# Optimization experiments

Hardware: AMD Instinct MI355X
Metric: run time of the kernel (lower is better)

Reference implementation:

```python
import jax, jax.numpy as jnp
import numpy as np
import math

B, N, E, H, DEPTH, MLP_RATIO, A = 8, 1024, 768, 12, 6, 4, 7
F = MLP_RATIO * E


def _get_attention_slopes(n):
    def p2(n):
        start = 2 ** (-2 ** (-(math.log2(n) - 3)))
        return [start * start ** i for i in range(n)]
    if math.log2(n).is_integer():
        return p2(n)
    c = 2 ** math.floor(math.log2(n))
    return p2(c) + _get_attention_slopes(2 * c)[0::2][: n - c]


def _ln(x, scale, bias, eps=1e-6):
    m = jnp.mean(x, axis=-1, keepdims=True)
    v = jnp.var(x, axis=-1, keepdims=True)
    return (x - m) * jax.lax.rsqrt(v + eps) * scale + bias


def setup_inputs() -> dict:
    key = jax.random.key(0)
    ks = jax.random.split(key, 8)
    s = 0.02
    return {
        "x": jax.random.normal(ks[0], (B, N, E), jnp.float32),
        "ln1_scale": jnp.ones((DEPTH, E), jnp.float32),
        "ln1_bias": jnp.zeros((DEPTH, E), jnp.float32),
        "wqkv": jax.random.normal(ks[1], (DEPTH, E, 3 * E), jnp.float32) * s,
        "bqkv": jnp.zeros((DEPTH, 3 * E), jnp.float32),
        "wo": jax.random.normal(ks[2], (DEPTH, E, E), jnp.float32) * s,
        "bo": jnp.zeros((DEPTH, E), jnp.float32),
        "ln2_scale": jnp.ones((DEPTH, E), jnp.float32),
        "ln2_bias": jnp.zeros((DEPTH, E), jnp.float32),
        "w1": jax.random.normal(ks[3], (DEPTH, E, F), jnp.float32) * s,
        "w2": jax.random.normal(ks[4], (DEPTH, F, E), jnp.float32) * s,
        "lnf_scale": jnp.ones((E,), jnp.float32),
        "lnf_bias": jnp.zeros((E,), jnp.float32),
        "head_w1": jax.random.normal(ks[5], (E, E), jnp.float32) * s,
        "head_b1": jnp.zeros((E,), jnp.float32),
        "head_w2": jax.random.normal(ks[6], (E, A), jnp.float32) * s,
    }


def reference(x, ln1_scale, ln1_bias, wqkv, bqkv, wo, bo, ln2_scale, ln2_bias, w1, w2, lnf_scale, lnf_bias, head_w1, head_b1, head_w2):
    b, n, e = x.shape
    h = H
    dh = e // h
    scale = dh ** (-0.5)
    # ALiBi bias: slopes[h] * key-position (exactly as original code computes it)
    slopes = jnp.asarray(_get_attention_slopes(h), x.dtype)
    pos_bias = slopes[None, :, None, None] * jnp.arange(n, dtype=x.dtype)[None, None, None, :]
    causal = jnp.tril(jnp.ones((n, n), bool))[None, None]  # [1,1,n,n]
    big_neg = jnp.finfo(x.dtype).min

    depth = ln1_scale.shape[0]
    for i in range(depth):
        y = _ln(x, ln1_scale[i], ln1_bias[i])
        qkv = y @ wqkv[i] + bqkv[i]
        q, k, v = jnp.split(qkv, 3, axis=-1)
        q = q.reshape(b, n, h, dh).transpose(0, 2, 1, 3)  # b h n d
        k = k.reshape(b, n, h, dh).transpose(0, 2, 1, 3)
        v = v.reshape(b, n, h, dh).transpose(0, 2, 1, 3)
        att = jnp.einsum('bhnd,bhmd->bhnm', q, k) * scale + pos_bias
        att = jnp.where(causal, att, big_neg)
        att = jax.nn.softmax(att, axis=-1)
        o = jnp.einsum('bhnm,bhmd->bhnd', att, v)
        o = o.transpose(0, 2, 1, 3).reshape(b, n, e)
        x = x + (o @ wo[i] + bo[i])
        y = _ln(x, ln2_scale[i], ln2_bias[i])
        y = jax.nn.gelu(y @ w1[i])  # flax default: tanh-approx gelu; FF has no bias
        x = x + y @ w2[i]
    x = _ln(x, lnf_scale, lnf_bias)
    actions = jax.nn.relu(x @ head_w1 + head_b1) @ head_w2
    return actions
```

## Files before the change

### kernel.cpp

```cpp
#include <hip/hip_runtime.h>
#include <hip/hip_bf16.h>
#include <cstdint>

#define DEV __device__ __forceinline__

typedef __bf16 bf16x8 __attribute__((ext_vector_type(8)));
typedef float f32x4 __attribute__((ext_vector_type(4)));
typedef unsigned short u16;
typedef u16 u16x8 __attribute__((ext_vector_type(8)));
typedef u16 u16x4 __attribute__((ext_vector_type(4)));
typedef uint32_t u32x2 __attribute__((ext_vector_type(2)));
typedef uint32_t u32x4 __attribute__((ext_vector_type(4)));

DEV u16 f2bf(float f) {
  union { float f; uint32_t u; } a; a.f = f;
  uint32_t u = a.u + 0x7fffu + ((a.u >> 16) & 1u);
  return (u16)(u >> 16);
}
DEV float b2f(u16 v) {
  union { uint32_t u; float f; } a; a.u = ((uint32_t)v) << 16;
  return a.f;
}

DEV float fexp2(float x) {
#if __has_builtin(__builtin_amdgcn_exp2f)
  return __builtin_amdgcn_exp2f(x);
#else
  return __expf(x * 0.69314718056f);
#endif
}

DEV uint32_t cvtpk(float lo, float hi) {
  uint32_t r;
  asm("v_cvt_pk_bf16_f32 %0, %1, %2" : "=v"(r) : "v"(lo), "v"(hi));
  return r;
}

DEV void gload16(const void* g, void* lds) {
  __builtin_amdgcn_global_load_lds((__attribute__((address_space(1))) void*)g,
                                   (__attribute__((address_space(3))) void*)lds,
                                   16, 0, 0);
}

struct TMat { const float* src; u16* dst; int K; int N; int t0; };
struct TArgs { TMat m[26]; int nmat; };

__global__ __launch_bounds__(256) void transpose_all(TArgs args) {
  __shared__ float tile[64][65];
  const int bid = blockIdx.x;
  int i = 0;
  #pragma unroll 1
  for (int t = 1; t < args.nmat; ++t) if (bid >= args.m[t].t0) i = t;
  const TMat mm = args.m[i];
  const int tid = bid - mm.t0;
  const int ntx = mm.N >> 6;
  const int tx = tid % ntx, ty = tid / ntx;
  const int n0 = tx * 64, k0 = ty * 64;
  const int c = threadIdx.x & 63, r0 = threadIdx.x >> 6;
  #pragma unroll
  for (int s = 0; s < 16; ++s) {
    int r = r0 + s * 4;
    tile[r][c] = mm.src[(size_t)(k0 + r) * mm.N + n0 + c];
  }
  __syncthreads();
  #pragma unroll
  for (int s = 0; s < 16; ++s) {
    int rr = r0 + s * 4;
    mm.dst[(size_t)(n0 + rr) * mm.K + k0 + c] = f2bf(tile[c][rr]);
  }
}

__global__ __launch_bounds__(256) void f2b_kernel(const float4* __restrict__ in,
                                                  u32x4* __restrict__ out, int n8) {
  const int i = blockIdx.x * 256 + threadIdx.x;
  if (i >= n8) return;
  float4 a = in[2 * i], b = in[2 * i + 1];
  u32x4 o;
  o[0] = cvtpk(a.x, a.y); o[1] = cvtpk(a.z, a.w);
  o[2] = cvtpk(b.x, b.y); o[3] = cvtpk(b.z, b.w);
  out[i] = o;
}

__global__ __launch_bounds__(256) void ln_kernel(const u16* __restrict__ x,
                                                 const float* __restrict__ sc,
                                                 const float* __restrict__ bi,
                                                 u16* __restrict__ y, int Mtok) {
  const int bid = blockIdx.x;
  const int tok = ((bid & 7) << 10) + ((bid >> 3) << 2) + (threadIdx.x >> 6);
  const int l = threadIdx.x & 63;
  if (tok >= Mtok) return;
  const u16* row = x + (size_t)tok * 768;
  u16x8 v0 = *(const u16x8*)(row + l * 8);
  u16x4 v1 = *(const u16x4*)(row + 512 + l * 4);
  float f[12];
  #pragma unroll
  for (int i = 0; i < 8; ++i) f[i] = b2f(v0[i]);
  #pragma unroll
  for (int i = 0; i < 4; ++i) f[8 + i] = b2f(v1[i]);
  float s = 0.f, q = 0.f;
  #pragma unroll
  for (int i = 0; i < 12; ++i) { s += f[i]; q += f[i] * f[i]; }
  #pragma unroll
  for (int off = 1; off < 64; off <<= 1) { s += __shfl_xor(s, off); q += __shfl_xor(q, off); }
  const float mean = s * (1.f / 768.f);
  const float var = q * (1.f / 768.f) - mean * mean;
  const float r = rsqrtf(var + 1e-6f);
  float4 s0 = *(const float4*)(sc + l * 8);
  float4 s1 = *(const float4*)(sc + l * 8 + 4);
  float4 s2 = *(const float4*)(sc + 512 + l * 4);
  float4 b0 = *(const float4*)(bi + l * 8);
  float4 b1 = *(const float4*)(bi + l * 8 + 4);
  float4 b2 = *(const float4*)(bi + 512 + l * 4);
  float g[12];
  g[0] = (f[0]-mean)*r*s0.x + b0.x;  g[1] = (f[1]-mean)*r*s0.y + b0.y;
  g[2] = (f[2]-mean)*r*s0.z + b0.z;  g[3] = (f[3]-mean)*r*s0.w + b0.w;
  g[4] = (f[4]-mean)*r*s1.x + b1.x;  g[5] = (f[5]-mean)*r*s1.y + b1.y;
  g[6] = (f[6]-mean)*r*s1.z + b1.z;  g[7] = (f[7]-mean)*r*s1.w + b1.w;
  g[8] = (f[8]-mean)*r*s2.x + b2.x;  g[9] = (f[9]-mean)*r*s2.y + b2.y;
  g[10] = (f[10]-mean)*r*s2.z + b2.z; g[11] = (f[11]-mean)*r*s2.w + b2.w;
  u16* yr = y + (size_t)tok * 768;
  u32x4 o;
  o[0] = cvtpk(g[0], g[1]); o[1] = cvtpk(g[2], g[3]);
  o[2] = cvtpk(g[4], g[5]); o[3] = cvtpk(g[6], g[7]);
  *(u32x4*)(yr + l * 8) = o;
  u32x2 o2; o2[0] = cvtpk(g[8], g[9]); o2[1] = cvtpk(g[10], g[11]);
  *(u32x2*)(yr + 512 + l * 4) = o2;
}

enum { EPI_BF16 = 0, EPI_RESID = 1, EPI_GELU = 2, EPI_RELU = 3 };

__global__ __launch_bounds__(256, 2) void gemm128(
    const u16* __restrict__ A, const u16* __restrict__ Bt,
    const float* __restrict__ bias, const u16* __restrict__ residB,
    u16* __restrict__ outB, int N, int K, int nxb, int epi) {
  __shared__ u16 smem[32768];
  const int tid = threadIdx.x;
  const int w = tid >> 6, l = tid & 63;

  const int nwg = gridDim.x;
  const int flat = blockIdx.x;
  const int wg = (flat & 7) * (nwg >> 3) + (flat >> 3);
  const int bx = wg % nxb, by = wg / nxb;
  const int m0 = by << 7, n0 = bx << 7;

  const int wr = (w >> 1) << 6, wc = (w & 1) << 6;
  const int cl = l & 15, g = l >> 4;
  f32x4 acc[4][4] = {};

  const int lrow = l >> 3;
  const int scol = ((l & 7) ^ lrow) << 3;
  const u16* agp = A  + (size_t)(m0 + (w << 5) + lrow) * K + scol;
  const u16* bgp = Bt + (size_t)(n0 + (w << 5) + lrow) * K + scol;
  const int ldso = w << 11;
  const int nkt = K >> 6;

  #pragma unroll
  for (int q = 0; q < 4; ++q) {
    gload16(agp + (size_t)(q * 8) * K, &smem[ldso + (q << 9)]);
    gload16(bgp + (size_t)(q * 8) * K, &smem[16384 + ldso + (q << 9)]);
  }

  const int sw = cl & 7;
  for (int kt = 0; kt < nkt; ++kt) {
    const int cur = kt & 1;
    if (kt + 1 < nkt) {
      const size_t koff = (size_t)(kt + 1) << 6;
      const int nb = (cur ^ 1) << 13;
      #pragma unroll
      for (int q = 0; q < 4; ++q) {
        gload16(agp + koff + (size_t)(q * 8) * K, &smem[nb + ldso + (q << 9)]);
        gload16(bgp + koff + (size_t)(q * 8) * K, &smem[16384 + nb + ldso + (q << 9)]);
      }
      asm volatile("s_waitcnt vmcnt(8)" ::: "memory");
    } else {
      asm volatile("s_waitcnt vmcnt(0)" ::: "memory");
    }
    __builtin_amdgcn_s_barrier();
    __builtin_amdgcn_sched_barrier(0);
    const u16* Ab = &smem[cur << 13];
    const u16* Bb = &smem[16384 + (cur << 13)];
    #pragma unroll
    for (int ks = 0; ks < 2; ++ks) {
      bf16x8 af[4], bfr[4];
      const int ps = (((ks << 2) | g) ^ sw) << 3;
      #pragma unroll
      for (int mt = 0; mt < 4; ++mt)
        af[mt] = *(const bf16x8*)(Ab + ((wr + mt * 16 + cl) << 6) + ps);
      #pragma unroll
      for (int nt = 0; nt < 4; ++nt)
        bfr[nt] = *(const bf16x8*)(Bb + ((wc + nt * 16 + cl) << 6) + ps);
      #pragma unroll
      for (int mt = 0; mt < 4; ++mt)
        #pragma unroll
        for (int nt = 0; nt < 4; ++nt)
          acc[mt][nt] = __builtin_amdgcn_mfma_f32_16x16x32_bf16(af[mt], bfr[nt], acc[mt][nt], 0, 0, 0);
    }
    asm volatile("s_waitcnt lgkmcnt(0)" ::: "memory");
    __builtin_amdgcn_s_barrier();
  }

  float* scr = (float*)smem + w * 1056;
  const int rg = g << 2;
  const int er = l >> 3;
  const int ec0 = (l & 7) << 3;
  #pragma unroll
  for (int mt = 0; mt < 4; ++mt) {
    #pragma unroll
    for (int nt = 0; nt < 4; ++nt)
      #pragma unroll
      for (int j = 0; j < 4; ++j)
        scr[(rg + j) * 66 + nt * 16 + cl] = acc[mt][nt][j];
    #pragma unroll
    for (int t = 0; t < 2; ++t) {
      const int r = (t << 3) + er;
      const int grow = m0 + wr + mt * 16 + r;
      const int gcol = n0 + wc + ec0;
      float v[8];
      #pragma unroll
      for (int u = 0; u < 8; ++u) v[u] = scr[r * 66 + ec0 + u];
      if (bias) {
        #pragma unroll
        for (int u = 0; u < 8; ++u) v[u] += bias[gcol + u];
      }
      if (epi == EPI_RESID) {
        u16x8 rv = *(const u16x8*)(residB + (size_t)grow * N + gcol);
        #pragma unroll
        for (int u = 0; u < 8; ++u) v[u] += b2f(rv[u]);
      } else if (epi == EPI_GELU) {
        #pragma unroll
        for (int u = 0; u < 8; ++u) {
          const float x = v[u];
          const float e = __expf(-(1.5957691216f * x + 0.0713548163f * x * x * x));
          v[u] = x / (1.f + e);
        }
      } else if (epi == EPI_RELU) {
        #pragma unroll
        for (int u = 0; u < 8; ++u) v[u] = fmaxf(v[u], 0.f);
      }
      u32x4 ov;
      ov[0] = cvtpk(v[0], v[1]); ov[1] = cvtpk(v[2], v[3]);
      ov[2] = cvtpk(v[4], v[5]); ov[3] = cvtpk(v[6], v[7]);
      u32x4* op = (u32x4*)(outB + (size_t)grow * N + gcol);
      if (epi == EPI_BF16 || epi == EPI_GELU)
        __builtin_nontemporal_store(ov, op);
      else
        *op = ov;
    }
  }
}

__global__ __launch_bounds__(512, 2) void attn_kernel(const u16* __restrict__ qkv,
                                                      u16* __restrict__ o) {
  __shared__ u16 Ksm[2][4096];
  __shared__ u16 Vt[2][64][68];
  __shared__ u16 P[8][16][72];
  const int flat = blockIdx.x;
  const int b = flat & 7;
  const int rr = flat >> 3;
  const int h = rr >> 3;
  const int j = rr & 7;
  const int tid = threadIdx.x;
  const int w = tid >> 6, l = tid & 63;
  const int cl = l & 15, lg = l >> 4;
  const int qtile = (w < 4) ? j : 15 - j;
  const int q0 = qtile * 64 + (w & 3) * 16;
  const int rowg = q0 + cl;
  const float log2e = 1.44269504f;
  const float scale2 = 0.125f * log2e;
  const float slope = (h < 8) ? exp2f(-(float)(h + 1)) : exp2f(-0.5f - (float)(h - 8));
  const float slope2 = slope * log2e;
  const size_t rs_ = 2304;
  const size_t bbase = (size_t)b * 1024 * rs_;

  const u16* qp = qkv + bbase + (size_t)rowg * rs_ + h * 64 + lg * 8;
  bf16x8 qa0 = *(const bf16x8*)qp;
  bf16x8 qa1 = *(const bf16x8*)(qp + 32);

  float m_r = -1e30f, l_r = 0.f;
  f32x4 oacc[4];
  #pragma unroll
  for (int d = 0; d < 4; ++d) oacc[d] = (f32x4){0.f, 0.f, 0.f, 0.f};

  const u16* ksrc = qkv + bbase + (size_t)(tid >> 3) * rs_ + 768 + h * 64 +
                    (((tid & 7) ^ ((tid >> 3) & 7)) << 3);
  const int vd0 = w << 3;
  const u16* vbase = qkv + bbase + (size_t)l * rs_ + 1536 + h * 64 + vd0;

  const int nkv = 16 - j;
  gload16(ksrc, &Ksm[0][w << 9]);
  u16x8 vreg = *(const u16x8*)vbase;
  __syncthreads();

  const int sw = cl & 7;
  const int ps0 = (lg ^ sw) << 3;
  const int ps1 = ps0 ^ 32;

  for (int kv = 0; kv < nkv; ++kv) {
    const int buf = kv & 1;
    #pragma unroll
    for (int i = 0; i < 8; ++i) Vt[buf][vd0 + i][l] = vreg[i];
    u16x8 vnext = vreg;
    if (kv + 1 < nkv) {
      gload16(ksrc + (size_t)(kv + 1) * 64 * rs_, &Ksm[buf ^ 1][w << 9]);
      vnext = *(const u16x8*)(vbase + (size_t)(kv + 1) * 64 * rs_);
    }

    const bool active = (kv <= qtile);
    bf16x8 pa0, pa1;
    if (active) {
      const u16* Kb = &Ksm[buf][0];
      f32x4 pp[4];
      float pm = -3.0e38f;
      __builtin_amdgcn_s_setprio(1);
      #pragma unroll
      for (int nt = 0; nt < 4; ++nt) {
        const int row = nt * 16 + cl;
        bf16x8 bk0 = *(const bf16x8*)(Kb + (row << 6) + ps0);
        bf16x8 bk1 = *(const bf16x8*)(Kb + (row << 6) + ps1);
        f32x4 s = (f32x4){0.f, 0.f, 0.f, 0.f};
        s = __builtin_amdgcn_mfma_f32_16x16x32_bf16(bk0, qa0, s, 0, 0, 0);
        s = __builtin_amdgcn_mfma_f32_16x16x32_bf16(bk1, qa1, s, 0, 0, 0);
        const int kb = kv * 64 + nt * 16 + (lg << 2);
        #pragma unroll
        for (int jj = 0; jj < 4; ++jj) {
          const int colg = kb + jj;
          float v = s[jj] * scale2 + slope2 * (float)colg;
          pp[nt][jj] = (colg <= rowg) ? v : -3.0e38f;
        }
        pm = fmaxf(pm, fmaxf(fmaxf(pp[nt][0], pp[nt][1]),
                             fmaxf(pp[nt][2], pp[nt][3])));
      }
      __builtin_amdgcn_s_setprio(0);
      pm = fmaxf(pm, __shfl_xor(pm, 16));
      pm = fmaxf(pm, __shfl_xor(pm, 32));
      if (!__all(pm <= m_r + 11.54f)) {
        const float mnew = fmaxf(m_r, pm);
        const float al = fexp2(m_r - mnew);
        m_r = mnew;
        l_r *= al;
        float a4[4];
        #pragma unroll
        for (int jj = 0; jj < 4; ++jj) a4[jj] = __shfl(al, (lg << 2) + jj);
        #pragma unroll
        for (int d = 0; d < 4; ++d)
          #pragma unroll
          for (int jj = 0; jj < 4; ++jj) oacc[d][jj] *= a4[jj];
      }
      float rs = 0.f;
      #pragma unroll
      for (int nt = 0; nt < 4; ++nt) {
        #pragma unroll
        for (int jj = 0; jj < 4; ++jj) {
          float p = fexp2(pp[nt][jj] - m_r);
          pp[nt][jj] = p;
          rs += p;
        }
      }
      rs += __shfl_xor(rs, 16);
      rs += __shfl_xor(rs, 32);
      l_r += rs;
      #pragma unroll
      for (int nt = 0; nt < 4; ++nt) {
        u32x2 pr;
        pr[0] = cvtpk(pp[nt][0], pp[nt][1]);
        pr[1] = cvtpk(pp[nt][2], pp[nt][3]);
        *(u32x2*)&P[w][cl][nt * 16 + (lg << 2)] = pr;
      }
      pa0 = *(const bf16x8*)&P[w][cl][lg * 8];
      pa1 = *(const bf16x8*)&P[w][cl][32 + lg * 8];
    }

    __syncthreads();

    if (active) {
      __builtin_amdgcn_s_setprio(1);
      #pragma unroll
      for (int d = 0; d < 4; ++d) {
        bf16x8 bv0 = *(const bf16x8*)&Vt[buf][d * 16 + cl][lg * 8];
        bf16x8 bv1 = *(const bf16x8*)&Vt[buf][d * 16 + cl][32 + lg * 8];
        oacc[d] = __builtin_amdgcn_mfma_f32_16x16x32_bf16(pa0, bv0, oacc[d], 0, 0, 0);
        oacc[d] = __builtin_amdgcn_mfma_f32_16x16x32_bf16(pa1, bv1, oacc[d], 0, 0, 0);
      }
      __builtin_amdgcn_s_setprio(0);
    }
    vreg = vnext;
  }

  const float linv = 1.f / l_r;
  float i4[4];
  #pragma unroll
  for (int jj = 0; jj < 4; ++jj) i4[jj] = __shfl(linv, (lg << 2) + jj);
  u16* op = o + ((size_t)b * 1024 + q0) * 768 + h * 64;
  #pragma unroll
  for (int d = 0; d < 4; ++d)
    #pragma unroll
    for (int jj = 0; jj < 4; ++jj)
      op[(size_t)((lg << 2) + jj) * 768 + d * 16 + cl] = f2bf(oacc[d][jj] * i4[jj]);
}

__global__ __launch_bounds__(256) void head2_kernel(const u16* __restrict__ act,
                                                    const float* __restrict__ w,
                                                    float* __restrict__ out, int Mtok) {
  const int bid = blockIdx.x;
  const int tok = ((bid & 7) << 10) + ((bid >> 3) << 2) + (threadIdx.x >> 6);
  const int l = threadIdx.x & 63;
  if (tok >= Mtok) return;
  float s[7] = {0.f, 0.f, 0.f, 0.f, 0.f, 0.f, 0.f};
  const u16* ar = act + (size_t)tok * 768;
  #pragma unroll
  for (int i = 0; i < 12; ++i) {
    const int k = l + i * 64;
    const float a = b2f(ar[k]);
    #pragma unroll
    for (int j = 0; j < 7; ++j) s[j] += a * w[k * 7 + j];
  }
  #pragma unroll
  for (int off = 32; off; off >>= 1)
    #pragma unroll
    for (int j = 0; j < 7; ++j) s[j] += __shfl_down(s[j], off);
  if (l == 0) {
    #pragma unroll
    for (int j = 0; j < 7; ++j) out[(size_t)tok * 7 + j] = s[j];
  }
}

extern "C" void kernel_launch(void* const* d_in, const int* in_sizes, int n_in,
                              void* d_out, int out_size, void* d_ws, size_t ws_size,
                              hipStream_t stream) {
  const float* x_in = (const float*)d_in[0];
  const float* ln1s = (const float*)d_in[1];
  const float* ln1b = (const float*)d_in[2];
  const float* wqkv = (const float*)d_in[3];
  const float* bqkv = (const float*)d_in[4];
  const float* wo   = (const float*)d_in[5];
  const float* bo   = (const float*)d_in[6];
  const float* ln2s = (const float*)d_in[7];
  const float* ln2b = (const float*)d_in[8];
  const float* w1   = (const float*)d_in[9];
  const float* w2   = (const float*)d_in[10];
  const float* lnfs = (const float*)d_in[11];
  const float* lnfb = (const float*)d_in[12];
  const float* hw1  = (const float*)d_in[13];
  const float* hb1  = (const float*)d_in[14];
  const float* hw2  = (const float*)d_in[15];
  float* out = (float*)d_out;

  const int Mtok = 8192, E = 768, E3 = 2304, F = 3072, DEPTH = 6;

  char* ws = (char*)d_ws;
  size_t off = 0;
  auto alloc = [&](size_t bytes) -> char* {
    char* p = ws + off; off += (bytes + 255) & ~(size_t)255; return p;
  };
  u16*  wqkvt = (u16*)alloc((size_t)DEPTH * E3 * E * 2);
  u16*  wot   = (u16*)alloc((size_t)DEPTH * E * E * 2);
  u16*  w1t   = (u16*)alloc((size_t)DEPTH * F * E * 2);
  u16*  w2t   = (u16*)alloc((size_t)DEPTH * E * F * 2);
  u16*  hw1t  = (u16*)alloc((size_t)E * E * 2);
  u16*  xb    = (u16*)alloc((size_t)Mtok * E * 2);
  u16*  yb    = (u16*)alloc((size_t)Mtok * E * 2);
  u16*  big   = (u16*)alloc((size_t)Mtok * F * 2);
  (void)ws_size; (void)in_sizes; (void)n_in; (void)out_size;

  TArgs ta; int nm = 0; int t0 = 0;
  auto add = [&](const float* s, u16* d, int K, int N) {
    ta.m[nm].src = s; ta.m[nm].dst = d; ta.m[nm].K = K; ta.m[nm].N = N; ta.m[nm].t0 = t0;
    t0 += (N / 64) * (K / 64); ++nm;
  };
  for (int i = 0; i < DEPTH; ++i) add(wqkv + (size_t)i * E * E3, wqkvt + (size_t)i * E3 * E, E, E3);
  for (int i = 0; i < DEPTH; ++i) add(wo + (size_t)i * E * E, wot + (size_t)i * E * E, E, E);
  for (int i = 0; i < DEPTH; ++i) add(w1 + (size_t)i * E * F, w1t + (size_t)i * F * E, E, F);
  for (int i = 0; i < DEPTH; ++i) add(w2 + (size_t)i * F * E, w2t + (size_t)i * E * F, F, E);
  add(hw1, hw1t, E, E);
  ta.nmat = nm;
  transpose_all<<<t0, 256, 0, stream>>>(ta);

  f2b_kernel<<<(Mtok * E / 8 + 255) / 256, 256, 0, stream>>>(
      (const float4*)x_in, (u32x4*)xb, Mtok * E / 8);

  u16* qkvb = big;
  for (int i = 0; i < DEPTH; ++i) {
    ln_kernel<<<Mtok / 4, 256, 0, stream>>>(xb, ln1s + i * E, ln1b + i * E, yb, Mtok);
    gemm128<<<18 * 64, 256, 0, stream>>>(yb, wqkvt + (size_t)i * E3 * E, bqkv + (size_t)i * E3,
                                         nullptr, qkvb, E3, E, 18, EPI_BF16);
    attn_kernel<<<768, 512, 0, stream>>>(qkvb, yb);
    gemm128<<<6 * 64, 256, 0, stream>>>(yb, wot + (size_t)i * E * E, bo + (size_t)i * E,
                                        xb, xb, E, E, 6, EPI_RESID);
    ln_kernel<<<Mtok / 4, 256, 0, stream>>>(xb, ln2s + i * E, ln2b + i * E, yb, Mtok);
    gemm128<<<24 * 64, 256, 0, stream>>>(yb, w1t + (size_t)i * F * E, nullptr,
                                         nullptr, big, F, E, 24, EPI_GELU);
    gemm128<<<6 * 64, 256, 0, stream>>>(big, w2t + (size_t)i * E * F, nullptr,
                                        xb, xb, E, F, 6, EPI_RESID);
  }
  ln_kernel<<<Mtok / 4, 256, 0, stream>>>(xb, lnfs, lnfb, yb, Mtok);
  gemm128<<<6 * 64, 256, 0, stream>>>(yb, hw1t, hb1, nullptr, big,
                                      E, E, 6, EPI_RELU);
  head2_kernel<<<Mtok / 4, 256, 0, stream>>>(big, hw2, out, Mtok);
}
```

Measured before the change: 1.410 ms.

## Fold LayerNorm into GEMM epilogues via precomputed weight column sums

Replaces the LayerNorm kernels that wrote normalized bf16 activations with a small row-stats kernel (mean, rstd). The LN scale is folded into the transposed weights, and per-column sums of scaled weights and of bias-weighted weights are computed with atomics during weight preparation. The GEMM then consumes raw x and applies (acc - mean*cs)*rstd + bW in its epilogue. This removes one full activation write and read per LayerNorm, at the cost of numerical differences from mean subtraction after bf16 accumulation and extra atomics in the transpose. The transpose kernel also switches to vectorized float4 loads and packed stores.

```diff
diff --git a/kernel.cpp b/kernel.cpp
--- a/kernel.cpp
+++ b/kernel.cpp
@@ -42,8 +42,9 @@
                                    16, 0, 0);
 }
 
-struct TMat { const float* src; u16* dst; int K; int N; int t0; };
-struct TArgs { TMat m[26]; int nmat; };
+struct TMat { const float* src; u16* dst; float* cs; float* bW;
+              const float* sc; const float* bi; int K; int N; int t0; };
+struct TArgs { TMat m[25]; int nmat; };
 
 __global__ __launch_bounds__(256) void transpose_all(TArgs args) {
   __shared__ float tile[64][65];
@@ -52,21 +53,42 @@
   #pragma unroll 1
   for (int t = 1; t < args.nmat; ++t) if (bid >= args.m[t].t0) i = t;
   const TMat mm = args.m[i];
-  const int tid = bid - mm.t0;
+  const int tid = threadIdx.x;
+  const int tix = bid - mm.t0;
   const int ntx = mm.N >> 6;
-  const int tx = tid % ntx, ty = tid / ntx;
-  const int n0 = tx * 64, k0 = ty * 64;
-  const int c = threadIdx.x & 63, r0 = threadIdx.x >> 6;
-  #pragma unroll
-  for (int s = 0; s < 16; ++s) {
-    int r = r0 + s * 4;
-    tile[r][c] = mm.src[(size_t)(k0 + r) * mm.N + n0 + c];
+  const int n0 = (tix % ntx) << 6, k0 = (tix / ntx) << 6;
+  const int lr = tid >> 4, lc4 = (tid & 15) << 2;
+  #pragma unroll
+  for (int p = 0; p < 4; ++p) {
+    const int r = lr + p * 16;
+    *(float4*)&tile[r][lc4] =
+        *(const float4*)(mm.src + (size_t)(k0 + r) * mm.N + n0 + lc4);
   }
   __syncthreads();
-  #pragma unroll
-  for (int s = 0; s < 16; ++s) {
-    int rr = r0 + s * 4;
-    mm.dst[(size_t)(n0 + rr) * mm.K + k0 + c] = f2bf(tile[c][rr]);
+  if (mm.cs && tid < 64) {
+    float s1 = 0.f, s2 = 0.f;
+    #pragma unroll 1
+    for (int r = 0; r < 64; ++r) {
+      const float v = tile[r][tid];
+      s1 += mm.sc[k0 + r] * v;
+      s2 += mm.bi[k0 + r] * v;
+    }
+    atomicAdd(mm.cs + n0 + tid, s1);
+    atomicAdd(mm.bW + n0 + tid, s2);
+  }
+  const int wn = tid >> 4, wk4 = (tid & 15) << 2;
+  float scv[4];
+  #pragma unroll
+  for (int u = 0; u < 4; ++u) scv[u] = mm.sc ? mm.sc[k0 + wk4 + u] : 1.f;
+  #pragma unroll
+  for (int p = 0; p < 4; ++p) {
+    const int n = wn + p * 16;
+    const float v0 = tile[wk4][n] * scv[0];
+    const float v1 = tile[wk4 + 1][n] * scv[1];
+    const float v2 = tile[wk4 + 2][n] * scv[2];
+    const float v3 = tile[wk4 + 3][n] * scv[3];
+    u32x2 o; o[0] = cvtpk(v0, v1); o[1] = cvtpk(v2, v3);
+    *(u32x2*)(mm.dst + (size_t)(n0 + n) * mm.K + k0 + wk4) = o;
   }
 }
 
@@ -81,10 +103,8 @@
   out[i] = o;
 }
 
-__global__ __launch_bounds__(256) void ln_kernel(const u16* __restrict__ x,
-                                                 const float* __restrict__ sc,
-                                                 const float* __restrict__ bi,
-                                                 u16* __restrict__ y, int Mtok) {
+__global__ __launch_bounds__(256) void rowstats(const u16* __restrict__ x,
+                                                float2* __restrict__ rs, int Mtok) {
   const int bid = blockIdx.x;
   const int tok = ((bid & 7) << 10) + ((bid >> 3) << 2) + (threadIdx.x >> 6);
   const int l = threadIdx.x & 63;
@@ -92,47 +112,29 @@
   const u16* row = x + (size_t)tok * 768;
   u16x8 v0 = *(const u16x8*)(row + l * 8);
   u16x4 v1 = *(const u16x4*)(row + 512 + l * 4);
-  float f[12];
-  #pragma unroll
-  for (int i = 0; i < 8; ++i) f[i] = b2f(v0[i]);
-  #pragma unroll
-  for (int i = 0; i < 4; ++i) f[8 + i] = b2f(v1[i]);
   float s = 0.f, q = 0.f;
   #pragma unroll
-  for (int i = 0; i < 12; ++i) { s += f[i]; q += f[i] * f[i]; }
+  for (int i = 0; i < 8; ++i) { float f = b2f(v0[i]); s += f; q += f * f; }
+  #pragma unroll
+  for (int i = 0; i < 4; ++i) { float f = b2f(v1[i]); s += f; q += f * f; }
   #pragma unroll
   for (int off = 1; off < 64; off <<= 1) { s += __shfl_xor(s, off); q += __shfl_xor(q, off); }
-  const float mean = s * (1.f / 768.f);
-  const float var = q * (1.f / 768.f) - mean * mean;
-  const float r = rsqrtf(var + 1e-6f);
-  float4 s0 = *(const float4*)(sc + l * 8);
-  float4 s1 = *(const float4*)(sc + l * 8 + 4);
-  float4 s2 = *(const float4*)(sc + 512 + l * 4);
-  float4 b0 = *(const float4*)(bi + l * 8);
-  float4 b1 = *(const float4*)(bi + l * 8 + 4);
-  float4 b2 = *(const float4*)(bi + 512 + l * 4);
-  float g[12];
-  g[0] = (f[0]-mean)*r*s0.x + b0.x;  g[1] = (f[1]-mean)*r*s0.y + b0.y;
-  g[2] = (f[2]-mean)*r*s0.z + b0.z;  g[3] = (f[3]-mean)*r*s0.w + b0.w;
-  g[4] = (f[4]-mean)*r*s1.x + b1.x;  g[5] = (f[5]-mean)*r*s1.y + b1.y;
-  g[6] = (f[6]-mean)*r*s1.z + b1.z;  g[7] = (f[7]-mean)*r*s1.w + b1.w;
-  g[8] = (f[8]-mean)*r*s2.x + b2.x;  g[9] = (f[9]-mean)*r*s2.y + b2.y;
-  g[10] = (f[10]-mean)*r*s2.z + b2.z; g[11] = (f[11]-mean)*r*s2.w + b2.w;
-  u16* yr = y + (size_t)tok * 768;
-  u32x4 o;
-  o[0] = cvtpk(g[0], g[1]); o[1] = cvtpk(g[2], g[3]);
-  o[2] = cvtpk(g[4], g[5]); o[3] = cvtpk(g[6], g[7]);
-  *(u32x4*)(yr + l * 8) = o;
-  u32x2 o2; o2[0] = cvtpk(g[8], g[9]); o2[1] = cvtpk(g[10], g[11]);
-  *(u32x2*)(yr + 512 + l * 4) = o2;
-}
-
-enum { EPI_BF16 = 0, EPI_RESID = 1, EPI_GELU = 2, EPI_RELU = 3 };
+  if (l == 0) {
+    const float mean = s * (1.f / 768.f);
+    const float var = q * (1.f / 768.f) - mean * mean;
+    float2 o; o.x = mean; o.y = rsqrtf(var + 1e-6f);
+    rs[tok] = o;
+  }
+}
+
+enum { EPI_LN = 0, EPI_RESID = 1, EPI_LNGELU = 2, EPI_LNRELU = 3 };
 
 __global__ __launch_bounds__(256, 2) void gemm128(
     const u16* __restrict__ A, const u16* __restrict__ Bt,
     const float* __restrict__ bias, const u16* __restrict__ residB,
-    u16* __restrict__ outB, int N, int K, int nxb, int epi) {
+    u16* __restrict__ outB, const float2* __restrict__ rstat,
+    const float* __restrict__ cs, const float* __restrict__ bW,
+    int N, int K, int nxb, int epi) {
   __shared__ u16 smem[32768];
   const int tid = threadIdx.x;
   const int w = tid >> 6, l = tid & 63;
@@ -218,30 +220,34 @@
       float v[8];
       #pragma unroll
       for (int u = 0; u < 8; ++u) v[u] = scr[r * 66 + ec0 + u];
-      if (bias) {
-        #pragma unroll
-        for (int u = 0; u < 8; ++u) v[u] += bias[gcol + u];
-      }
       if (epi == EPI_RESID) {
+        if (bias) {
+          #pragma unroll
+          for (int u = 0; u < 8; ++u) v[u] += bias[gcol + u];
+        }
         u16x8 rv = *(const u16x8*)(residB + (size_t)grow * N + gcol);
         #pragma unroll
         for (int u = 0; u < 8; ++u) v[u] += b2f(rv[u]);
-      } else if (epi == EPI_GELU) {
+      } else {
+        const float2 st = rstat[grow];
         #pragma unroll
         for (int u = 0; u < 8; ++u) {
-          const float x = v[u];
-          const float e = __expf(-(1.5957691216f * x + 0.0713548163f * x * x * x));
-          v[u] = x / (1.f + e);
+          float x = (v[u] - st.x * cs[gcol + u]) * st.y + bW[gcol + u];
+          if (bias) x += bias[gcol + u];
+          if (epi == EPI_LNGELU) {
+            const float e = __expf(-(1.5957691216f * x + 0.0713548163f * x * x * x));
+            x = x / (1.f + e);
+          } else if (epi == EPI_LNRELU) {
+            x = fmaxf(x, 0.f);
+          }
+          v[u] = x;
         }
-      } else if (epi == EPI_RELU) {
-        #pragma unroll
-        for (int u = 0; u < 8; ++u) v[u] = fmaxf(v[u], 0.f);
       }
       u32x4 ov;
       ov[0] = cvtpk(v[0], v[1]); ov[1] = cvtpk(v[2], v[3]);
       ov[2] = cvtpk(v[4], v[5]); ov[3] = cvtpk(v[6], v[7]);
       u32x4* op = (u32x4*)(outB + (size_t)grow * N + gcol);
-      if (epi == EPI_BF16 || epi == EPI_GELU)
+      if (epi == EPI_LN || epi == EPI_LNGELU)
         __builtin_nontemporal_store(ov, op);
       else
         *op = ov;
@@ -457,21 +463,40 @@
   u16*  w1t   = (u16*)alloc((size_t)DEPTH * F * E * 2);
   u16*  w2t   = (u16*)alloc((size_t)DEPTH * E * F * 2);
   u16*  hw1t  = (u16*)alloc((size_t)E * E * 2);
+  const int ncs = DEPTH * E3 * 2 + DEPTH * F * 2 + E * 2;
+  float* csbuf = (float*)alloc((size_t)ncs * 4);
+  float* csq = csbuf;            float* bWq = csq + DEPTH * E3;
+  float* csw = bWq + DEPTH * E3; float* bWw = csw + DEPTH * F;
+  float* csh = bWw + DEPTH * F;  float* bWh = csh + E;
+  float2* rs = (float2*)alloc((size_t)Mtok * 8);
   u16*  xb    = (u16*)alloc((size_t)Mtok * E * 2);
   u16*  yb    = (u16*)alloc((size_t)Mtok * E * 2);
   u16*  big   = (u16*)alloc((size_t)Mtok * F * 2);
   (void)ws_size; (void)in_sizes; (void)n_in; (void)out_size;
 
+  hipMemsetAsync(csbuf, 0, (size_t)ncs * 4, stream);
+
   TArgs ta; int nm = 0; int t0 = 0;
-  auto add = [&](const float* s, u16* d, int K, int N) {
-    ta.m[nm].src = s; ta.m[nm].dst = d; ta.m[nm].K = K; ta.m[nm].N = N; ta.m[nm].t0 = t0;
+  auto add = [&](const float* s, u16* d, int K, int N,
+                 float* cs, float* bW, const float* sc, const float* bi) {
+    ta.m[nm].src = s; ta.m[nm].dst = d; ta.m[nm].cs = cs; ta.m[nm].bW = bW;
+    ta.m[nm].sc = sc; ta.m[nm].bi = bi; ta.m[nm].K = K; ta.m[nm].N = N;
+    ta.m[nm].t0 = t0;
     t0 += (N / 64) * (K / 64); ++nm;
   };
-  for (int i = 0; i < DEPTH; ++i) add(wqkv + (size_t)i * E * E3, wqkvt + (size_t)i * E3 * E, E, E3);
-  for (int i = 0; i < DEPTH; ++i) add(wo + (size_t)i * E * E, wot + (size_t)i * E * E, E, E);
-  for (int i = 0; i < DEPTH; ++i) add(w1 + (size_t)i * E * F, w1t + (size_t)i * F * E, E, F);
-  for (int i = 0; i < DEPTH; ++i) add(w2 + (size_t)i * F * E, w2t + (size_t)i * E * F, F, E);
-  add(hw1, hw1t, E, E);
+  for (int i = 0; i < DEPTH; ++i)
+    add(wqkv + (size_t)i * E * E3, wqkvt + (size_t)i * E3 * E, E, E3,
+        csq + i * E3, bWq + i * E3, ln1s + i * E, ln1b + i * E);
+  for (int i = 0; i < DEPTH; ++i)
+    add(wo + (size_t)i * E * E, wot + (size_t)i * E * E, E, E,
+        nullptr, nullptr, nullptr, nullptr);
+  for (int i = 0; i < DEPTH; ++i)
+    add(w1 + (size_t)i * E * F, w1t + (size_t)i * F * E, E, F,
+        csw + i * F, bWw + i * F, ln2s + i * E, ln2b + i * E);
+  for (int i = 0; i < DEPTH; ++i)
+    add(w2 + (size_t)i * F * E, w2t + (size_t)i * E * F, F, E,
+        nullptr, nullptr, nullptr, nullptr);
+  add(hw1, hw1t, E, E, csh, bWh, lnfs, lnfb);
   ta.nmat = nm;
   transpose_all<<<t0, 256, 0, stream>>>(ta);
 
@@ -480,20 +505,28 @@
 
   u16* qkvb = big;
   for (int i = 0; i < DEPTH; ++i) {
-    ln_kernel<<<Mtok / 4, 256, 0, stream>>>(xb, ln1s + i * E, ln1b + i * E, yb, Mtok);
-    gemm128<<<18 * 64, 256, 0, stream>>>(yb, wqkvt + (size_t)i * E3 * E, bqkv + (size_t)i * E3,
-                                         nullptr, qkvb, E3, E, 18, EPI_BF16);
+    rowstats<<<Mtok / 4, 256, 0, stream>>>(xb, rs, Mtok);
+    gemm128<<<18 * 64, 256, 0, stream>>>(xb, wqkvt + (size_t)i * E3 * E,
+                                         bqkv + (size_t)i * E3, nullptr, qkvb,
+                                         rs, csq + i * E3, bWq + i * E3,
+                                         E3, E, 18, EPI_LN);
     attn_kernel<<<768, 512, 0, stream>>>(qkvb, yb);
-    gemm128<<<6 * 64, 256, 0, stream>>>(yb, wot + (size_t)i * E * E, bo + (size_t)i * E,
-                                        xb, xb, E, E, 6, EPI_RESID);
-    ln_kernel<<<Mtok / 4, 256, 0, stream>>>(xb, ln2s + i * E, ln2b + i * E, yb, Mtok);
-    gemm128<<<24 * 64, 256, 0, stream>>>(yb, w1t + (size_t)i * F * E, nullptr,
-                                         nullptr, big, F, E, 24, EPI_GELU);
-    gemm128<<<6 * 64, 256, 0, stream>>>(big, w2t + (size_t)i * E * F, nullptr,
-                                        xb, xb, E, F, 6, EPI_RESID);
-  }
-  ln_kernel<<<Mtok / 4, 256, 0, stream>>>(xb, lnfs, lnfb, yb, Mtok);
-  gemm128<<<6 * 64, 256, 0, stream>>>(yb, hw1t, hb1, nullptr, big,
-                                      E, E, 6, EPI_RELU);
+    gemm128<<<6 * 64, 256, 0, stream>>>(yb, wot + (size_t)i * E * E,
+                                        bo + (size_t)i * E, xb, xb,
+                                        nullptr, nullptr, nullptr,
+                                        E, E, 6, EPI_RESID);
+    rowstats<<<Mtok / 4, 256, 0, stream>>>(xb, rs, Mtok);
+    gemm128<<<24 * 64, 256, 0, stream>>>(xb, w1t + (size_t)i * F * E,
+                                         nullptr, nullptr, big,
+                                         rs, csw + i * F, bWw + i * F,
+                                         F, E, 24, EPI_LNGELU);
+    gemm128<<<6 * 64, 256, 0, stream>>>(big, w2t + (size_t)i * E * F,
+                                        nullptr, xb, xb,
+                                        nullptr, nullptr, nullptr,
+                                        E, F, 6, EPI_RESID);
+  }
+  rowstats<<<Mtok / 4, 256, 0, stream>>>(xb, rs, Mtok);
+  gemm128<<<6 * 64, 256, 0, stream>>>(xb, hw1t, hb1, nullptr, big,
+                                      rs, csh, bWh, E, E, 6, EPI_LNRELU);
   head2_kernel<<<Mtok / 4, 256, 0, stream>>>(big, hw2, out, Mtok);
 }
```

New measurement: 1.911 ms. 35.5% more time.
